# Kernel optimization log

Hardware: AMD Instinct MI355X
Metric: run time of the kernel (lower is better)

The kernel has to match this reference:

```python
import jax, jax.numpy as jnp
import numpy as np

HID, OUT, EMB, NL = 256, 128, 1024, 4
NR, NP_, NM = 16384, 40000, 30000
E = 200000
NTYPES = 3  # lin_nodes keys: protein, molecule, reaction


def setup_inputs() -> dict:
    key = jax.random.key(0)
    ks = jax.random.split(key, 32)
    f32 = jnp.float32
    inp = {}
    inp["x_reaction"] = jax.random.normal(ks[0], (NR, EMB), f32)
    inp["x_protein"] = jax.random.normal(ks[1], (NP_, EMB), f32)
    inp["x_molecule"] = jax.random.normal(ks[2], (NM, EMB), f32)
    inp["ei_p2r_src"] = jax.random.randint(ks[3], (E,), 0, NP_, jnp.int32)
    inp["ei_p2r_dst"] = jax.random.randint(ks[4], (E,), 0, NR, jnp.int32)
    inp["ei_m2r_src"] = jax.random.randint(ks[5], (E,), 0, NM, jnp.int32)
    inp["ei_m2r_dst"] = jax.random.randint(ks[6], (E,), 0, NR, jnp.int32)
    inp["ei_r2p_src"] = jax.random.randint(ks[7], (E,), 0, NR, jnp.int32)
    inp["ei_r2p_dst"] = jax.random.randint(ks[8], (E,), 0, NP_, jnp.int32)
    inp["ei_r2m_src"] = jax.random.randint(ks[9], (E,), 0, NR, jnp.int32)
    inp["ei_r2m_dst"] = jax.random.randint(ks[10], (E,), 0, NM, jnp.int32)
    inp["output_notes_opt"] = jax.random.normal(ks[11], (NR, EMB), f32)
    inp["output_types"] = jax.random.randint(ks[12], (NR,), 0, NTYPES, jnp.int32)
    s = 0.02
    # layer 0 SAGE params (lazy in_dim = EMB), one set per edge type (4 edge types)
    inp["Wl0"] = jax.random.normal(ks[13], (4, EMB, HID), f32) * s
    inp["Wr0"] = jax.random.normal(ks[14], (4, EMB, HID), f32) * s
    inp["bl0"] = jnp.zeros((4, HID), f32)
    # layers 1..3 SAGE params (in_dim = HID)
    inp["Wl"] = jax.random.normal(ks[15], (NL - 1, 4, HID, HID), f32) * s
    inp["Wr"] = jax.random.normal(ks[16], (NL - 1, 4, HID, HID), f32) * s
    inp["bl"] = jnp.zeros((NL - 1, 4, HID), f32)
    inp["W_reaction"] = jax.random.normal(ks[17], (HID, OUT), f32) * s
    inp["b_reaction"] = jnp.zeros((OUT,), f32)
    inp["W_nodes"] = jax.random.normal(ks[18], (NTYPES, EMB, OUT), f32) * s
    inp["b_nodes"] = jnp.zeros((NTYPES, OUT), f32)
    return inp


def _sage(x_src, x_dst, src, dst, n_dst, Wl, bl, Wr):
    # PyG SAGEConv (aggr='mean'): lin_l(mean_{j->i} x_j) + lin_r(x_i); lin_l has bias.
    g = x_src[src]                                              # [E, d] gather
    s = jax.ops.segment_sum(g, dst, num_segments=n_dst)          # [n_dst, d]
    cnt = jax.ops.segment_sum(jnp.ones((src.shape[0],), x_src.dtype), dst, num_segments=n_dst)
    mean = s / jnp.maximum(cnt, 1.0)[:, None]
    return mean @ Wl + bl + x_dst @ Wr


def _hetero_layer(xr, xp, xm, edges, Wl, bl, Wr):
    # HeteroConv(aggr='sum'): sum SAGE outputs per destination node type.
    (ps, pd), (ms, md), (rps, rpd), (rms, rmd) = edges
    new_r = (_sage(xp, xr, ps, pd, NR, Wl[0], bl[0], Wr[0])
             + _sage(xm, xr, ms, md, NR, Wl[1], bl[1], Wr[1]))
    new_p = _sage(xr, xp, rps, rpd, NP_, Wl[2], bl[2], Wr[2])
    new_m = _sage(xr, xm, rms, rmd, NM, Wl[3], bl[3], Wr[3])
    return new_r, new_p, new_m


def reference(x_reaction, x_protein, x_molecule,
              ei_p2r_src, ei_p2r_dst, ei_m2r_src, ei_m2r_dst,
              ei_r2p_src, ei_r2p_dst, ei_r2m_src, ei_r2m_dst,
              output_notes_opt, output_types,
              Wl0, bl0, Wr0, Wl, bl, Wr,
              W_reaction, b_reaction, W_nodes, b_nodes):
    edges = ((ei_p2r_src, ei_p2r_dst), (ei_m2r_src, ei_m2r_dst),
             (ei_r2p_src, ei_r2p_dst), (ei_r2m_src, ei_r2m_dst))
    xr, xp, xm = _hetero_layer(x_reaction, x_protein, x_molecule, edges, Wl0, bl0, Wr0)
    for l in range(NL - 1):
        xr, xp, xm = _hetero_layer(xr, xp, xm, edges, Wl[l], bl[l], Wr[l])
    reaction_out = xr @ W_reaction + b_reaction                  # [NR, OUT]
    # lin_nodes[t](v) per output node: project with all type linears, select by type id
    projs = jnp.einsum('ke,ted->ktd', output_notes_opt, W_nodes) + b_nodes[None]  # [NR, T, OUT]
    node_out = jnp.take_along_axis(projs, output_types[:, None, None].astype(jnp.int32), axis=1)[:, 0, :]
    # cosine similarity along dim=1, torch-style eps clamp on the norm product
    num = jnp.sum(reaction_out * node_out, axis=-1)
    den = jnp.maximum(jnp.linalg.norm(reaction_out, axis=-1) * jnp.linalg.norm(node_out, axis=-1), 1e-8)
    return (num / den + 1.0) * 0.5
```

## Files before the change

### kernel.cpp

```cpp
#include <hip/hip_runtime.h>
#include <math.h>
#include <stdint.h>

#define NR_ 16384
#define NP2_ 40000
#define NM_ 30000
#define NE_ 200000
#define EMB_ 1024
#define HID_ 256
#define OUTD_ 128

typedef __attribute__((ext_vector_type(8))) short bf16x8;
typedef __attribute__((ext_vector_type(4))) float f32x4;
typedef __attribute__((ext_vector_type(8))) unsigned short us8;

__device__ __forceinline__ unsigned short f2bf(float f) {
    uint32_t u = __builtin_bit_cast(uint32_t, f);
    u = (u + 0x7FFFu + ((u >> 16) & 1u)) >> 16;
    return (unsigned short)u;
}
__device__ __forceinline__ float bf2f(unsigned short u) {
    uint32_t v = ((uint32_t)u) << 16;
    return __builtin_bit_cast(float, v);
}

struct Csr4 {
    const int* src[4]; const int* dst[4];
    int* offs[4]; int* cur[4]; int* csr[4];
    int n[4];
};
__global__ void k_zero4(Csr4 c) {
    int y = blockIdx.y;
    int i = blockIdx.x * 256 + threadIdx.x;
    if (i < c.n[y]) c.cur[y][i] = 0;
}
__global__ void k_deg4(Csr4 c) {
    int y = blockIdx.y;
    int i = blockIdx.x * 256 + threadIdx.x;
    if (i < NE_) atomicAdd(&c.cur[y][c.dst[y][i]], 1);
}
__global__ void k_scanA(Csr4 c, int* __restrict__ csum) {
    int y = blockIdx.y;
    int n = c.n[y];
    int ch = blockIdx.x;
    int nch = (n + 1023) >> 10;
    if (ch >= nch) return;
    const int* deg = c.cur[y];
    int* offs = c.offs[y];
    __shared__ int ts[256];
    int base = ch << 10;
    int t = threadIdx.x;
    int v[4];
    int s = 0;
    #pragma unroll
    for (int k = 0; k < 4; ++k) {
        int i = base + t * 4 + k;
        v[k] = (i < n) ? deg[i] : 0;
        s += v[k];
    }
    ts[t] = s;
    __syncthreads();
    for (int st = 1; st < 256; st <<= 1) {
        int x = ts[t];
        int xo = (t >= st) ? ts[t - st] : 0;
        __syncthreads();
        ts[t] = x + xo;
        __syncthreads();
    }
    int run = (t > 0) ? ts[t - 1] : 0;
    #pragma unroll
    for (int k = 0; k < 4; ++k) {
        int i = base + t * 4 + k;
        if (i < n) offs[i] = run;
        run += v[k];
    }
    if (t == 255) csum[y * 40 + ch] = ts[255];
}
__global__ void k_scanB(Csr4 c, int* __restrict__ csum) {
    int y = threadIdx.x;
    if (y < 4) {
        int n = c.n[y];
        int nch = (n + 1023) >> 10;
        int acc = 0;
        for (int i = 0; i < nch; ++i) {
            int v = csum[y * 40 + i];
            csum[y * 40 + i] = acc;
            acc += v;
        }
        c.offs[y][n] = acc;
    }
}
__global__ void k_scanC(Csr4 c, const int* __restrict__ csum) {
    int y = blockIdx.y;
    int i = blockIdx.x * 256 + threadIdx.x;
    if (i < c.n[y]) {
        int v = c.offs[y][i] + csum[y * 40 + (i >> 10)];
        c.offs[y][i] = v;
        c.cur[y][i] = v;
    }
}
__global__ void k_scatter4(Csr4 c) {
    int y = blockIdx.y;
    int i = blockIdx.x * 256 + threadIdx.x;
    if (i < NE_) {
        int d = c.dst[y][i];
        int p = atomicAdd(&c.cur[y][d], 1);
        c.csr[y][p] = c.src[y][i];
    }
}

struct WItem { const float* a; const float* b; unsigned short* dst; int k; int n; };
struct WBatch { WItem it[32]; };
__global__ void k_wconvT(WBatch wb) {
    WItem w = wb.it[blockIdx.y];
    int total = w.k * w.n;
    int kmask = w.k - 1;
    int shift = (w.k == 1024) ? 10 : 8;
    for (int idx = blockIdx.x * 256 + threadIdx.x; idx < total; idx += gridDim.x * 256) {
        int k = idx & kmask, n = idx >> shift;
        float v = w.a[(size_t)k * w.n + n];
        if (w.b) v += w.b[(size_t)k * w.n + n];
        w.dst[idx] = f2bf(v);
    }
}

template <bool OBF, bool AF32>
__global__ __launch_bounds__(256, 3) void k_gemm(
    const void* __restrict__ Av, int lda,
    const unsigned short* __restrict__ Bt,
    void* __restrict__ Cv, int ldc, const float* __restrict__ bias,
    int M, int K)
{
    __shared__ __align__(16) unsigned short As[128 * 64];
    __shared__ __align__(16) unsigned short Bs[128 * 64];
    const int tid = threadIdx.x;
    const int lane = tid & 63;
    int nwg = gridDim.x * gridDim.y;
    int o = blockIdx.y * gridDim.x + blockIdx.x;
    int q = nwg >> 3, r = nwg & 7;
    int xcd = o & 7, j = o >> 3;
    int wg = (xcd < r ? xcd * (q + 1) : r * (q + 1) + (xcd - r) * q) + j;
    const int bm = (wg / gridDim.y) * 128;
    const int bn = (wg % gridDim.y) * 128;
    const int wave = tid >> 6;
    const int wr = (wave >> 1) * 64;
    const int wc = (wave & 1) * 64;
    const int frow = lane & 15;
    const int fkc = lane >> 4;
    f32x4 acc[4][4] = {};

    for (int k0 = 0; k0 < K; k0 += 64) {
        #pragma unroll
        for (int i = 0; i < 4; ++i) {
            int c = tid + i * 256;
            int row = c >> 3, kc = c & 7;
            int srck = k0 + ((kc ^ (row & 7)) << 3);
            int ga = min(bm + row, M - 1);
            if constexpr (AF32) {
                const float* Af = (const float*)Av + (size_t)ga * lda + srck;
                float4 a0 = *(const float4*)Af;
                float4 a1 = *(const float4*)(Af + 4);
                us8 oo;
                oo[0] = f2bf(a0.x); oo[1] = f2bf(a0.y); oo[2] = f2bf(a0.z); oo[3] = f2bf(a0.w);
                oo[4] = f2bf(a1.x); oo[5] = f2bf(a1.y); oo[6] = f2bf(a1.z); oo[7] = f2bf(a1.w);
                *(us8*)(As + (size_t)c * 8) = oo;
            } else {
                __builtin_amdgcn_global_load_lds(
                    (const __attribute__((address_space(1))) unsigned int*)((const unsigned short*)Av + (size_t)ga * lda + srck),
                    (__attribute__((address_space(3))) unsigned int*)(As + (size_t)c * 8), 16, 0, 0);
            }
            __builtin_amdgcn_global_load_lds(
                (const __attribute__((address_space(1))) unsigned int*)(Bt + (size_t)(bn + row) * K + srck),
                (__attribute__((address_space(3))) unsigned int*)(Bs + (size_t)c * 8), 16, 0, 0);
        }
        __syncthreads();
        #pragma unroll
        for (int kk = 0; kk < 2; ++kk) {
            bf16x8 af[4], bfr[4];
            #pragma unroll
            for (int m = 0; m < 4; ++m) {
                int row = wr + m * 16 + frow;
                int kc = kk * 4 + fkc;
                af[m] = *(const bf16x8*)(As + (size_t)((row << 3) + (kc ^ (row & 7))) * 8);
            }
            #pragma unroll
            for (int n = 0; n < 4; ++n) {
                int row = wc + n * 16 + frow;
                int kc = kk * 4 + fkc;
                bfr[n] = *(const bf16x8*)(Bs + (size_t)((row << 3) + (kc ^ (row & 7))) * 8);
            }
            #pragma unroll
            for (int m = 0; m < 4; ++m)
                #pragma unroll
                for (int n = 0; n < 4; ++n)
                    acc[m][n] = __builtin_amdgcn_mfma_f32_16x16x32_bf16(bfr[n], af[m], acc[m][n], 0, 0, 0);
        }
        __syncthreads();
    }

    const int ccol0 = (lane >> 4) << 2;
    #pragma unroll
    for (int m = 0; m < 4; ++m) {
        int row = bm + wr + m * 16 + frow;
        if (row < M) {
            #pragma unroll
            for (int n = 0; n < 4; ++n) {
                int col = bn + wc + n * 16 + ccol0;
                f32x4 v = acc[m][n];
                if (bias) {
                    v[0] += bias[col + 0];
                    v[1] += bias[col + 1];
                    v[2] += bias[col + 2];
                    v[3] += bias[col + 3];
                }
                if constexpr (OBF) {
                    ushort4 oo;
                    oo.x = f2bf(v[0]); oo.y = f2bf(v[1]); oo.z = f2bf(v[2]); oo.w = f2bf(v[3]);
                    *(ushort4*)((unsigned short*)Cv + (size_t)row * ldc + col) = oo;
                } else {
                    *(float4*)((float*)Cv + (size_t)row * ldc + col) = make_float4(v[0], v[1], v[2], v[3]);
                }
            }
        }
    }
}

__global__ __launch_bounds__(256) void k_aggw(const int* __restrict__ offs,
                                              const int* __restrict__ csr,
                                              const unsigned short* __restrict__ proj, int ldp,
                                              const float* __restrict__ bias,
                                              unsigned short* __restrict__ outx, int ldo,
                                              int ndst) {
    int node = blockIdx.x * 4 + (threadIdx.x >> 6);
    int lane = threadIdx.x & 63;
    if (node >= ndst) return;
    int beg = offs[node], end = offs[node + 1];
    float s0 = 0.f, s1 = 0.f, s2 = 0.f, s3 = 0.f;
    const unsigned short* base = proj + lane * 4;
    int e = beg;
    for (; e + 1 < end; e += 2) {
        int i0 = csr[e], i1 = csr[e + 1];
        ushort4 u0 = *(const ushort4*)(base + (size_t)i0 * ldp);
        ushort4 u1 = *(const ushort4*)(base + (size_t)i1 * ldp);
        s0 += bf2f(u0.x) + bf2f(u1.x);
        s1 += bf2f(u0.y) + bf2f(u1.y);
        s2 += bf2f(u0.z) + bf2f(u1.z);
        s3 += bf2f(u0.w) + bf2f(u1.w);
    }
    if (e < end) {
        ushort4 u = *(const ushort4*)(base + (size_t)csr[e] * ldp);
        s0 += bf2f(u.x); s1 += bf2f(u.y); s2 += bf2f(u.z); s3 += bf2f(u.w);
    }
    float inv = 1.f / fmaxf((float)(end - beg), 1.f);
    float4 b4 = ((const float4*)bias)[lane];
    size_t o = (size_t)node * ldo + lane * 4;
    ushort4 cur = *(const ushort4*)(outx + o);
    ushort4 w;
    w.x = f2bf(bf2f(cur.x) + s0 * inv + b4.x);
    w.y = f2bf(bf2f(cur.y) + s1 * inv + b4.y);
    w.z = f2bf(bf2f(cur.z) + s2 * inv + b4.z);
    w.w = f2bf(bf2f(cur.w) + s3 * inv + b4.w);
    *(ushort4*)(outx + o) = w;
}

__global__ __launch_bounds__(256) void k_agg2w(const int* __restrict__ offsA,
                                               const int* __restrict__ csrA,
                                               const unsigned short* __restrict__ projA, int ldpA,
                                               const float* __restrict__ biasA,
                                               const int* __restrict__ offsB,
                                               const int* __restrict__ csrB,
                                               const unsigned short* __restrict__ projB, int ldpB,
                                               const float* __restrict__ biasB,
                                               unsigned short* __restrict__ outx, int ldo,
                                               int ndst) {
    int node = blockIdx.x * 4 + (threadIdx.x >> 6);
    int lane = threadIdx.x & 63;
    if (node >= ndst) return;
    float a0 = 0.f, a1 = 0.f, a2 = 0.f, a3 = 0.f;
    int begA = offsA[node], endA = offsA[node + 1];
    const unsigned short* baseA = projA + lane * 4;
    int e = begA;
    for (; e + 1 < endA; e += 2) {
        int i0 = csrA[e], i1 = csrA[e + 1];
        ushort4 u0 = *(const ushort4*)(baseA + (size_t)i0 * ldpA);
        ushort4 u1 = *(const ushort4*)(baseA + (size_t)i1 * ldpA);
        a0 += bf2f(u0.x) + bf2f(u1.x);
        a1 += bf2f(u0.y) + bf2f(u1.y);
        a2 += bf2f(u0.z) + bf2f(u1.z);
        a3 += bf2f(u0.w) + bf2f(u1.w);
    }
    if (e < endA) {
        ushort4 u = *(const ushort4*)(baseA + (size_t)csrA[e] * ldpA);
        a0 += bf2f(u.x); a1 += bf2f(u.y); a2 += bf2f(u.z); a3 += bf2f(u.w);
    }
    float b0 = 0.f, b1 = 0.f, b2 = 0.f, b3 = 0.f;
    int begB = offsB[node], endB = offsB[node + 1];
    const unsigned short* baseB = projB + lane * 4;
    e = begB;
    for (; e + 1 < endB; e += 2) {
        int i0 = csrB[e], i1 = csrB[e + 1];
        ushort4 u0 = *(const ushort4*)(baseB + (size_t)i0 * ldpB);
        ushort4 u1 = *(const ushort4*)(baseB + (size_t)i1 * ldpB);
        b0 += bf2f(u0.x) + bf2f(u1.x);
        b1 += bf2f(u0.y) + bf2f(u1.y);
        b2 += bf2f(u0.z) + bf2f(u1.z);
        b3 += bf2f(u0.w) + bf2f(u1.w);
    }
    if (e < endB) {
        ushort4 u = *(const ushort4*)(baseB + (size_t)csrB[e] * ldpB);
        b0 += bf2f(u.x); b1 += bf2f(u.y); b2 += bf2f(u.z); b3 += bf2f(u.w);
    }
    float invA = 1.f / fmaxf((float)(endA - begA), 1.f);
    float invB = 1.f / fmaxf((float)(endB - begB), 1.f);
    float4 bA = ((const float4*)biasA)[lane];
    float4 bB = ((const float4*)biasB)[lane];
    size_t o = (size_t)node * ldo + lane * 4;
    ushort4 cur = *(const ushort4*)(outx + o);
    ushort4 w;
    w.x = f2bf(bf2f(cur.x) + a0 * invA + bA.x + b0 * invB + bB.x);
    w.y = f2bf(bf2f(cur.y) + a1 * invA + bA.y + b1 * invB + bB.y);
    w.z = f2bf(bf2f(cur.z) + a2 * invA + bA.z + b2 * invB + bB.z);
    w.w = f2bf(bf2f(cur.w) + a3 * invA + bA.w + b3 * invB + bB.w);
    *(ushort4*)(outx + o) = w;
}

__global__ __launch_bounds__(256) void k_cos(const float* __restrict__ ro,
                                             const float* __restrict__ pr,
                                             const int* __restrict__ types,
                                             float* __restrict__ out, int nr) {
    int row = blockIdx.x * 4 + (threadIdx.x >> 6);
    int lane = threadIdx.x & 63;
    if (row >= nr) return;
    int t = types[row];
    float2 r = ((const float2*)(ro + (size_t)row * OUTD_))[lane];
    float2 nn = ((const float2*)(pr + (size_t)row * 384 + t * OUTD_))[lane];
    float num = r.x * nn.x + r.y * nn.y;
    float d1 = r.x * r.x + r.y * r.y;
    float d2 = nn.x * nn.x + nn.y * nn.y;
    #pragma unroll
    for (int s = 1; s < 64; s <<= 1) {
        num += __shfl_xor(num, s);
        d1 += __shfl_xor(d1, s);
        d2 += __shfl_xor(d2, s);
    }
    if (lane == 0) out[row] = (num / fmaxf(sqrtf(d1) * sqrtf(d2), 1e-8f) + 1.f) * 0.5f;
}

extern "C" void kernel_launch(void* const* d_in, const int* in_sizes, int n_in,
                              void* d_out, int out_size, void* d_ws, size_t ws_size,
                              hipStream_t stream) {
    const float* x_r0 = (const float*)d_in[0];
    const float* x_p0 = (const float*)d_in[1];
    const float* x_m0 = (const float*)d_in[2];
    const int* e_src[4] = {(const int*)d_in[3], (const int*)d_in[5], (const int*)d_in[7], (const int*)d_in[9]};
    const int* e_dst[4] = {(const int*)d_in[4], (const int*)d_in[6], (const int*)d_in[8], (const int*)d_in[10]};
    const float* notes = (const float*)d_in[11];
    const int* types = (const int*)d_in[12];
    const float* Wl0 = (const float*)d_in[13];
    const float* Wr0 = (const float*)d_in[14];
    const float* bl0 = (const float*)d_in[15];
    const float* WlL = (const float*)d_in[16];
    const float* WrL = (const float*)d_in[17];
    const float* blL = (const float*)d_in[18];
    const float* Wre = (const float*)d_in[19];
    const float* bre = (const float*)d_in[20];
    const float* Wn  = (const float*)d_in[21];
    const float* bn  = (const float*)d_in[22];
    float* out = (float*)d_out;

    uintptr_t base = (uintptr_t)d_ws;
    auto alloc = [&](size_t bytes) -> void* {
        uintptr_t p = (base + 255) & ~(uintptr_t)255;
        base = p + bytes;
        return (void*)p;
    };
    unsigned short* Rb[2] = {(unsigned short*)alloc((size_t)NR_ * 768 * 2),
                             (unsigned short*)alloc((size_t)NR_ * 768 * 2)};
    unsigned short* Pb[2] = {(unsigned short*)alloc((size_t)NP2_ * 512 * 2),
                             (unsigned short*)alloc((size_t)NP2_ * 512 * 2)};
    unsigned short* Mb[2] = {(unsigned short*)alloc((size_t)NM_ * 512 * 2),
                             (unsigned short*)alloc((size_t)NM_ * 512 * 2)};
    float* ro = (float*)alloc((size_t)NR_ * OUTD_ * 4);
    float* pr = (float*)alloc((size_t)NR_ * 384 * 4);
    unsigned short* wbf = (unsigned short*)alloc((size_t)4000000 * 2);
    int* csum = (int*)alloc(160 * 4);
    int nd[4] = {NR_, NR_, NP2_, NM_};
    Csr4 cs{};
    for (int t = 0; t < 4; ++t) {
        cs.src[t] = e_src[t]; cs.dst[t] = e_dst[t]; cs.n[t] = nd[t];
        cs.offs[t] = (int*)alloc(((size_t)nd[t] + 1) * 4);
        cs.cur[t]  = (int*)alloc((size_t)nd[t] * 4);
        cs.csr[t]  = (int*)alloc((size_t)NE_ * 4);
    }

    unsigned short *BR[4], *BP[4], *BM[4], *Bre, *Bn;
    {
        WBatch wb{};
        int cnt = 0;
        size_t woff = 0;
        auto add = [&](const float* a, const float* bb, int K, int N) -> unsigned short* {
            unsigned short* dst = wbf + woff;
            woff += (size_t)K * N;
            wb.it[cnt] = WItem{a, bb, dst, K, N};
            ++cnt;
            return dst;
        };
        const size_t w0 = (size_t)EMB_ * HID_;
        const size_t wl = (size_t)HID_ * HID_;
        for (int l = 0; l < 4; ++l) {
            int K = (l == 0) ? EMB_ : HID_;
            const float* Wr_ = (l == 0) ? Wr0 : WrL + (size_t)(l - 1) * 4 * wl;
            const float* Wl_ = (l == 0) ? Wl0 : WlL + (size_t)(l - 1) * 4 * wl;
            size_t ws_ = (l == 0) ? w0 : wl;
            BR[l] = add(Wr_ + 0 * ws_, Wr_ + 1 * ws_, K, HID_);
            add(Wl_ + 2 * ws_, nullptr, K, HID_);
            add(Wl_ + 3 * ws_, nullptr, K, HID_);
            BP[l] = add(Wr_ + 2 * ws_, nullptr, K, HID_);
            add(Wl_ + 0 * ws_, nullptr, K, HID_);
            BM[l] = add(Wr_ + 3 * ws_, nullptr, K, HID_);
            add(Wl_ + 1 * ws_, nullptr, K, HID_);
        }
        Bre = add(Wre, nullptr, HID_, OUTD_);
        Bn = add(Wn + 0 * (size_t)EMB_ * OUTD_, nullptr, EMB_, OUTD_);
        add(Wn + 1 * (size_t)EMB_ * OUTD_, nullptr, EMB_, OUTD_);
        add(Wn + 2 * (size_t)EMB_ * OUTD_, nullptr, EMB_, OUTD_);
        k_wconvT<<<dim3(128, cnt), 256, 0, stream>>>(wb);
    }

    k_zero4<<<dim3((NP2_ + 255) / 256, 4), 256, 0, stream>>>(cs);
    k_deg4<<<dim3((NE_ + 255) / 256, 4), 256, 0, stream>>>(cs);
    k_scanA<<<dim3(40, 4), 256, 0, stream>>>(cs, csum);
    k_scanB<<<1, 64, 0, stream>>>(cs, csum);
    k_scanC<<<dim3((NP2_ + 255) / 256, 4), 256, 0, stream>>>(cs, csum);
    k_scatter4<<<dim3((NE_ + 255) / 256, 4), 256, 0, stream>>>(cs);

    auto gemm_bf = [&](const unsigned short* A, int lda, const unsigned short* Bt,
                       unsigned short* C, int ldc, int M, int N, int K) {
        k_gemm<true, false><<<dim3((M + 127) / 128, N / 128), 256, 0, stream>>>(
            A, lda, Bt, C, ldc, nullptr, M, K);
    };
    auto gemm_f32a_bf = [&](const float* A, int lda, const unsigned short* Bt,
                            unsigned short* C, int ldc, int M, int N, int K) {
        k_gemm<true, true><<<dim3((M + 127) / 128, N / 128), 256, 0, stream>>>(
            A, lda, Bt, C, ldc, nullptr, M, K);
    };

    for (int l = 0; l < 4; ++l) {
        int K = (l == 0) ? EMB_ : HID_;
        unsigned short* R = Rb[l & 1];
        unsigned short* P = Pb[l & 1];
        unsigned short* M = Mb[l & 1];
        const float* bl_ = (l == 0) ? bl0 : blL + (size_t)(l - 1) * 4 * HID_;

        if (l == 0) {
            gemm_f32a_bf(x_r0, EMB_, BR[0], R, 768, NR_, 768, EMB_);
            gemm_f32a_bf(x_p0, EMB_, BP[0], P, 512, NP2_, 512, EMB_);
            gemm_f32a_bf(x_m0, EMB_, BM[0], M, 512, NM_, 512, EMB_);
        } else {
            gemm_bf(Rb[(l - 1) & 1], 768, BR[l], R, 768, NR_, 768, K);
            gemm_bf(Pb[(l - 1) & 1], 512, BP[l], P, 512, NP2_, 512, K);
            gemm_bf(Mb[(l - 1) & 1], 512, BM[l], M, 512, NM_, 512, K);
        }

        k_agg2w<<<(NR_ + 3) / 4, 256, 0, stream>>>(cs.offs[0], cs.csr[0], P + 256, 512, bl_ + 0 * HID_,
                                                   cs.offs[1], cs.csr[1], M + 256, 512, bl_ + 1 * HID_,
                                                   R, 768, NR_);
        k_aggw<<<(NP2_ + 3) / 4, 256, 0, stream>>>(cs.offs[2], cs.csr[2], R + 256, 768, bl_ + 2 * HID_, P, 512, NP2_);
        k_aggw<<<(NM_ + 3) / 4, 256, 0, stream>>>(cs.offs[3], cs.csr[3], R + 512, 768, bl_ + 3 * HID_, M, 512, NM_);
    }

    k_gemm<false, false><<<dim3((NR_ + 127) / 128, 1), 256, 0, stream>>>(
        Rb[1], 768, Bre, ro, OUTD_, bre, NR_, HID_);
    k_gemm<false, true><<<dim3((NR_ + 127) / 128, 3), 256, 0, stream>>>(
        notes, EMB_, Bn, pr, 384, bn, NR_, EMB_);
    k_cos<<<NR_ / 4, 256, 0, stream>>>(ro, pr, types, out, NR_);
}
```

Measured before the change: 887.9 us.

## Double-buffer LDS tiles in GEMM to overlap global loads with MFMA

The GEMM kernel now keeps two LDS buffers for the A and B tiles and prefetches the next K-tile while running MFMAs on the current one. This removes one barrier per iteration. For fp32 A inputs, the next tile is loaded into registers and converted to bf16 after the compute step. This doubles LDS use to 64KB and lowers the launch-bounds occupancy hint from 3 to 2 blocks, trading occupancy and register pressure for overlap.

New measurement: 936.2 us. 1.05x slower.

```diff
diff --git a/kernel.cpp b/kernel.cpp
--- a/kernel.cpp
+++ b/kernel.cpp
@@ -125,14 +125,14 @@
 }
 
 template <bool OBF, bool AF32>
-__global__ __launch_bounds__(256, 3) void k_gemm(
+__global__ __launch_bounds__(256, 2) void k_gemm(
     const void* __restrict__ Av, int lda,
     const unsigned short* __restrict__ Bt,
     void* __restrict__ Cv, int ldc, const float* __restrict__ bias,
     int M, int K)
 {
-    __shared__ __align__(16) unsigned short As[128 * 64];
-    __shared__ __align__(16) unsigned short Bs[128 * 64];
+    __shared__ __align__(16) unsigned short As[2][128 * 64];
+    __shared__ __align__(16) unsigned short Bs[2][128 * 64];
     const int tid = threadIdx.x;
     const int lane = tid & 63;
     int nwg = gridDim.x * gridDim.y;
@@ -148,54 +148,104 @@
     const int frow = lane & 15;
     const int fkc = lane >> 4;
     f32x4 acc[4][4] = {};
-
-    for (int k0 = 0; k0 < K; k0 += 64) {
-        #pragma unroll
-        for (int i = 0; i < 4; ++i) {
-            int c = tid + i * 256;
-            int row = c >> 3, kc = c & 7;
-            int srck = k0 + ((kc ^ (row & 7)) << 3);
-            int ga = min(bm + row, M - 1);
-            if constexpr (AF32) {
-                const float* Af = (const float*)Av + (size_t)ga * lda + srck;
-                float4 a0 = *(const float4*)Af;
-                float4 a1 = *(const float4*)(Af + 4);
-                us8 oo;
-                oo[0] = f2bf(a0.x); oo[1] = f2bf(a0.y); oo[2] = f2bf(a0.z); oo[3] = f2bf(a0.w);
-                oo[4] = f2bf(a1.x); oo[5] = f2bf(a1.y); oo[6] = f2bf(a1.z); oo[7] = f2bf(a1.w);
-                *(us8*)(As + (size_t)c * 8) = oo;
-            } else {
-                __builtin_amdgcn_global_load_lds(
-                    (const __attribute__((address_space(1))) unsigned int*)((const unsigned short*)Av + (size_t)ga * lda + srck),
-                    (__attribute__((address_space(3))) unsigned int*)(As + (size_t)c * 8), 16, 0, 0);
+    float4 ra0[4], ra1[4];
+    (void)ra0; (void)ra1;
+
+#define STAGE_AB(bufi, kk0) do {                                                           \
+    _Pragma("unroll")                                                                      \
+    for (int i = 0; i < 4; ++i) {                                                          \
+        int c = tid + i * 256, rw = c >> 3, kc = c & 7;                                    \
+        int srck = (kk0) + ((kc ^ (rw & 7)) << 3);                                         \
+        int ga = min(bm + rw, M - 1);                                                      \
+        __builtin_amdgcn_global_load_lds(                                                  \
+            (const __attribute__((address_space(1))) unsigned int*)((const unsigned short*)Av + (size_t)ga * lda + srck), \
+            (__attribute__((address_space(3))) unsigned int*)(&As[bufi][c * 8]), 16, 0, 0);\
+        __builtin_amdgcn_global_load_lds(                                                  \
+            (const __attribute__((address_space(1))) unsigned int*)(Bt + (size_t)(bn + rw) * K + srck), \
+            (__attribute__((address_space(3))) unsigned int*)(&Bs[bufi][c * 8]), 16, 0, 0);\
+    } } while (0)
+
+#define ALOAD(kk0) do {                                                                    \
+    _Pragma("unroll")                                                                      \
+    for (int i = 0; i < 4; ++i) {                                                          \
+        int c = tid + i * 256, rw = c >> 3, kc = c & 7;                                    \
+        int srck = (kk0) + ((kc ^ (rw & 7)) << 3);                                         \
+        int ga = min(bm + rw, M - 1);                                                      \
+        const float* Af = (const float*)Av + (size_t)ga * lda + srck;                      \
+        ra0[i] = *(const float4*)Af;                                                       \
+        ra1[i] = *(const float4*)(Af + 4);                                                 \
+    } } while (0)
+
+#define AWRITE(bufi) do {                                                                  \
+    _Pragma("unroll")                                                                      \
+    for (int i = 0; i < 4; ++i) {                                                          \
+        int c = tid + i * 256;                                                             \
+        us8 oo;                                                                            \
+        oo[0] = f2bf(ra0[i].x); oo[1] = f2bf(ra0[i].y);                                    \
+        oo[2] = f2bf(ra0[i].z); oo[3] = f2bf(ra0[i].w);                                    \
+        oo[4] = f2bf(ra1[i].x); oo[5] = f2bf(ra1[i].y);                                    \
+        oo[6] = f2bf(ra1[i].z); oo[7] = f2bf(ra1[i].w);                                    \
+        *(us8*)(&As[bufi][c * 8]) = oo;                                                    \
+    } } while (0)
+
+#define STAGE_B(bufi, kk0) do {                                                            \
+    _Pragma("unroll")                                                                      \
+    for (int i = 0; i < 4; ++i) {                                                          \
+        int c = tid + i * 256, rw = c >> 3, kc = c & 7;                                    \
+        int srck = (kk0) + ((kc ^ (rw & 7)) << 3);                                         \
+        __builtin_amdgcn_global_load_lds(                                                  \
+            (const __attribute__((address_space(1))) unsigned int*)(Bt + (size_t)(bn + rw) * K + srck), \
+            (__attribute__((address_space(3))) unsigned int*)(&Bs[bufi][c * 8]), 16, 0, 0);\
+    } } while (0)
+
+#define COMPUTE(bufi) do {                                                                 \
+    _Pragma("unroll")                                                                      \
+    for (int kk = 0; kk < 2; ++kk) {                                                       \
+        bf16x8 af[4], bfr[4];                                                              \
+        _Pragma("unroll")                                                                  \
+        for (int m = 0; m < 4; ++m) {                                                      \
+            int rw = wr + m * 16 + frow;                                                   \
+            int kc = kk * 4 + fkc;                                                         \
+            af[m] = *(const bf16x8*)(&As[bufi][((rw << 3) + (kc ^ (rw & 7))) * 8]);        \
+        }                                                                                  \
+        _Pragma("unroll")                                                                  \
+        for (int n = 0; n < 4; ++n) {                                                      \
+            int rw = wc + n * 16 + frow;                                                   \
+            int kc = kk * 4 + fkc;                                                         \
+            bfr[n] = *(const bf16x8*)(&Bs[bufi][((rw << 3) + (kc ^ (rw & 7))) * 8]);       \
+        }                                                                                  \
+        _Pragma("unroll")                                                                  \
+        for (int m = 0; m < 4; ++m)                                                        \
+            _Pragma("unroll")                                                              \
+            for (int n = 0; n < 4; ++n)                                                    \
+                acc[m][n] = __builtin_amdgcn_mfma_f32_16x16x32_bf16(bfr[n], af[m], acc[m][n], 0, 0, 0); \
+    } } while (0)
+
+    const int nt = K >> 6;
+    if constexpr (AF32) {
+        ALOAD(0);
+        STAGE_B(0, 0);
+        AWRITE(0);
+        __syncthreads();
+        for (int t = 0; t < nt; ++t) {
+            int bufi = t & 1;
+            if (t + 1 < nt) {
+                ALOAD((t + 1) << 6);
+                STAGE_B(bufi ^ 1, (t + 1) << 6);
             }
-            __builtin_amdgcn_global_load_lds(
-                (const __attribute__((address_space(1))) unsigned int*)(Bt + (size_t)(bn + row) * K + srck),
-                (__attribute__((address_space(3))) unsigned int*)(Bs + (size_t)c * 8), 16, 0, 0);
+            COMPUTE(bufi);
+            if (t + 1 < nt) AWRITE(bufi ^ 1);
+            __syncthreads();
         }
+    } else {
+        STAGE_AB(0, 0);
         __syncthreads();
-        #pragma unroll
-        for (int kk = 0; kk < 2; ++kk) {
-            bf16x8 af[4], bfr[4];
-            #pragma unroll
-            for (int m = 0; m < 4; ++m) {
-                int row = wr + m * 16 + frow;
-                int kc = kk * 4 + fkc;
-                af[m] = *(const bf16x8*)(As + (size_t)((row << 3) + (kc ^ (row & 7))) * 8);
-            }
-            #pragma unroll
-            for (int n = 0; n < 4; ++n) {
-                int row = wc + n * 16 + frow;
-                int kc = kk * 4 + fkc;
-                bfr[n] = *(const bf16x8*)(Bs + (size_t)((row << 3) + (kc ^ (row & 7))) * 8);
-            }
-            #pragma unroll
-            for (int m = 0; m < 4; ++m)
-                #pragma unroll
-                for (int n = 0; n < 4; ++n)
-                    acc[m][n] = __builtin_amdgcn_mfma_f32_16x16x32_bf16(bfr[n], af[m], acc[m][n], 0, 0, 0);
+        for (int t = 0; t < nt; ++t) {
+            int bufi = t & 1;
+            if (t + 1 < nt) STAGE_AB(bufi ^ 1, (t + 1) << 6);
+            COMPUTE(bufi);
+            __syncthreads();
         }
-        __syncthreads();
     }
 
     const int ccol0 = (lane >> 4) << 2;
@@ -223,6 +273,11 @@
             }
         }
     }
+#undef STAGE_AB
+#undef ALOAD
+#undef AWRITE
+#undef STAGE_B
+#undef COMPUTE
 }
 
 __global__ __launch_bounds__(256) void k_aggw(const int* __restrict__ offs,
```

## Batch per-layer node-type GEMMs into one grouped launch; unroll aggregation gathers by four

Applied to the files above, without the earlier changes.

The three per-layer projection GEMMs (reaction, protein, molecule) are merged into one grouped kernel. It takes a segment table and maps each workgroup to its segment through block-offset thresholds, which removes two launches per layer and lets tail tiles of one GEMM overlap with the next. The CSR mean-aggregation loops are also unrolled from two to four gathers per iteration so more loads are in flight. The cost is extra per-block segment selection and struct reads, and higher register use in the aggregation kernels.

Result: faster. 805.5 us (-9.3%).

```diff
diff --git a/kernel.cpp b/kernel.cpp
--- a/kernel.cpp
+++ b/kernel.cpp
@@ -124,24 +124,32 @@
     }
 }
 
+struct GSeg {
+    const void* A; const unsigned short* Bt; void* C; const float* bias;
+    int lda, ldc, M, K, ntn, blk0;
+};
+struct GBatch { GSeg s[3]; int b1, b2, tot; };
+
 template <bool OBF, bool AF32>
-__global__ __launch_bounds__(256, 3) void k_gemm(
-    const void* __restrict__ Av, int lda,
-    const unsigned short* __restrict__ Bt,
-    void* __restrict__ Cv, int ldc, const float* __restrict__ bias,
-    int M, int K)
-{
+__global__ __launch_bounds__(256, 3) void k_gemmb(GBatch gb) {
     __shared__ __align__(16) unsigned short As[128 * 64];
     __shared__ __align__(16) unsigned short Bs[128 * 64];
     const int tid = threadIdx.x;
     const int lane = tid & 63;
-    int nwg = gridDim.x * gridDim.y;
-    int o = blockIdx.y * gridDim.x + blockIdx.x;
+    int nwg = gb.tot;
+    int o = blockIdx.x;
     int q = nwg >> 3, r = nwg & 7;
     int xcd = o & 7, j = o >> 3;
     int wg = (xcd < r ? xcd * (q + 1) : r * (q + 1) + (xcd - r) * q) + j;
-    const int bm = (wg / gridDim.y) * 128;
-    const int bn = (wg % gridDim.y) * 128;
+    const int si = (wg >= gb.b1) + (wg >= gb.b2);
+    const GSeg sg = gb.s[si];
+    const int local = wg - sg.blk0;
+    const int bm = (local / sg.ntn) * 128;
+    const int bn = (local % sg.ntn) * 128;
+    const int lda = sg.lda, ldc = sg.ldc, M = sg.M, K = sg.K;
+    const unsigned short* __restrict__ Bt = sg.Bt;
+    const float* __restrict__ bias = sg.bias;
+
     const int wave = tid >> 6;
     const int wr = (wave >> 1) * 64;
     const int wc = (wave & 1) * 64;
@@ -157,7 +165,7 @@
             int srck = k0 + ((kc ^ (row & 7)) << 3);
             int ga = min(bm + row, M - 1);
             if constexpr (AF32) {
-                const float* Af = (const float*)Av + (size_t)ga * lda + srck;
+                const float* Af = (const float*)sg.A + (size_t)ga * lda + srck;
                 float4 a0 = *(const float4*)Af;
                 float4 a1 = *(const float4*)(Af + 4);
                 us8 oo;
@@ -166,7 +174,7 @@
                 *(us8*)(As + (size_t)c * 8) = oo;
             } else {
                 __builtin_amdgcn_global_load_lds(
-                    (const __attribute__((address_space(1))) unsigned int*)((const unsigned short*)Av + (size_t)ga * lda + srck),
+                    (const __attribute__((address_space(1))) unsigned int*)((const unsigned short*)sg.A + (size_t)ga * lda + srck),
                     (__attribute__((address_space(3))) unsigned int*)(As + (size_t)c * 8), 16, 0, 0);
             }
             __builtin_amdgcn_global_load_lds(
@@ -216,9 +224,9 @@
                 if constexpr (OBF) {
                     ushort4 oo;
                     oo.x = f2bf(v[0]); oo.y = f2bf(v[1]); oo.z = f2bf(v[2]); oo.w = f2bf(v[3]);
-                    *(ushort4*)((unsigned short*)Cv + (size_t)row * ldc + col) = oo;
+                    *(ushort4*)((unsigned short*)sg.C + (size_t)row * ldc + col) = oo;
                 } else {
-                    *(float4*)((float*)Cv + (size_t)row * ldc + col) = make_float4(v[0], v[1], v[2], v[3]);
+                    *(float4*)((float*)sg.C + (size_t)row * ldc + col) = make_float4(v[0], v[1], v[2], v[3]);
                 }
             }
         }
@@ -238,16 +246,18 @@
     float s0 = 0.f, s1 = 0.f, s2 = 0.f, s3 = 0.f;
     const unsigned short* base = proj + lane * 4;
     int e = beg;
-    for (; e + 1 < end; e += 2) {
-        int i0 = csr[e], i1 = csr[e + 1];
+    for (; e + 3 < end; e += 4) {
+        int i0 = csr[e], i1 = csr[e + 1], i2 = csr[e + 2], i3 = csr[e + 3];
         ushort4 u0 = *(const ushort4*)(base + (size_t)i0 * ldp);
         ushort4 u1 = *(const ushort4*)(base + (size_t)i1 * ldp);
-        s0 += bf2f(u0.x) + bf2f(u1.x);
-        s1 += bf2f(u0.y) + bf2f(u1.y);
-        s2 += bf2f(u0.z) + bf2f(u1.z);
-        s3 += bf2f(u0.w) + bf2f(u1.w);
-    }
-    if (e < end) {
+        ushort4 u2 = *(const ushort4*)(base + (size_t)i2 * ldp);
+        ushort4 u3 = *(const ushort4*)(base + (size_t)i3 * ldp);
+        s0 += bf2f(u0.x) + bf2f(u1.x) + bf2f(u2.x) + bf2f(u3.x);
+        s1 += bf2f(u0.y) + bf2f(u1.y) + bf2f(u2.y) + bf2f(u3.y);
+        s2 += bf2f(u0.z) + bf2f(u1.z) + bf2f(u2.z) + bf2f(u3.z);
+        s3 += bf2f(u0.w) + bf2f(u1.w) + bf2f(u2.w) + bf2f(u3.w);
+    }
+    for (; e < end; ++e) {
         ushort4 u = *(const ushort4*)(base + (size_t)csr[e] * ldp);
         s0 += bf2f(u.x); s1 += bf2f(u.y); s2 += bf2f(u.z); s3 += bf2f(u.w);
     }
@@ -280,16 +290,18 @@
     int begA = offsA[node], endA = offsA[node + 1];
     const unsigned short* baseA = projA + lane * 4;
     int e = begA;
-    for (; e + 1 < endA; e += 2) {
-        int i0 = csrA[e], i1 = csrA[e + 1];
+    for (; e + 3 < endA; e += 4) {
+        int i0 = csrA[e], i1 = csrA[e + 1], i2 = csrA[e + 2], i3 = csrA[e + 3];
         ushort4 u0 = *(const ushort4*)(baseA + (size_t)i0 * ldpA);
         ushort4 u1 = *(const ushort4*)(baseA + (size_t)i1 * ldpA);
-        a0 += bf2f(u0.x) + bf2f(u1.x);
-        a1 += bf2f(u0.y) + bf2f(u1.y);
-        a2 += bf2f(u0.z) + bf2f(u1.z);
-        a3 += bf2f(u0.w) + bf2f(u1.w);
-    }
-    if (e < endA) {
+        ushort4 u2 = *(const ushort4*)(baseA + (size_t)i2 * ldpA);
+        ushort4 u3 = *(const ushort4*)(baseA + (size_t)i3 * ldpA);
+        a0 += bf2f(u0.x) + bf2f(u1.x) + bf2f(u2.x) + bf2f(u3.x);
+        a1 += bf2f(u0.y) + bf2f(u1.y) + bf2f(u2.y) + bf2f(u3.y);
+        a2 += bf2f(u0.z) + bf2f(u1.z) + bf2f(u2.z) + bf2f(u3.z);
+        a3 += bf2f(u0.w) + bf2f(u1.w) + bf2f(u2.w) + bf2f(u3.w);
+    }
+    for (; e < endA; ++e) {
         ushort4 u = *(const ushort4*)(baseA + (size_t)csrA[e] * ldpA);
         a0 += bf2f(u.x); a1 += bf2f(u.y); a2 += bf2f(u.z); a3 += bf2f(u.w);
     }
@@ -297,16 +309,18 @@
     int begB = offsB[node], endB = offsB[node + 1];
     const unsigned short* baseB = projB + lane * 4;
     e = begB;
-    for (; e + 1 < endB; e += 2) {
-        int i0 = csrB[e], i1 = csrB[e + 1];
+    for (; e + 3 < endB; e += 4) {
+        int i0 = csrB[e], i1 = csrB[e + 1], i2 = csrB[e + 2], i3 = csrB[e + 3];
         ushort4 u0 = *(const ushort4*)(baseB + (size_t)i0 * ldpB);
         ushort4 u1 = *(const ushort4*)(baseB + (size_t)i1 * ldpB);
-        b0 += bf2f(u0.x) + bf2f(u1.x);
-        b1 += bf2f(u0.y) + bf2f(u1.y);
-        b2 += bf2f(u0.z) + bf2f(u1.z);
-        b3 += bf2f(u0.w) + bf2f(u1.w);
-    }
-    if (e < endB) {
+        ushort4 u2 = *(const ushort4*)(baseB + (size_t)i2 * ldpB);
+        ushort4 u3 = *(const ushort4*)(baseB + (size_t)i3 * ldpB);
+        b0 += bf2f(u0.x) + bf2f(u1.x) + bf2f(u2.x) + bf2f(u3.x);
+        b1 += bf2f(u0.y) + bf2f(u1.y) + bf2f(u2.y) + bf2f(u3.y);
+        b2 += bf2f(u0.z) + bf2f(u1.z) + bf2f(u2.z) + bf2f(u3.z);
+        b3 += bf2f(u0.w) + bf2f(u1.w) + bf2f(u2.w) + bf2f(u3.w);
+    }
+    for (; e < endB; ++e) {
         ushort4 u = *(const ushort4*)(baseB + (size_t)csrB[e] * ldpB);
         b0 += bf2f(u.x); b1 += bf2f(u.y); b2 += bf2f(u.z); b3 += bf2f(u.w);
     }
@@ -434,15 +448,12 @@
     k_scanC<<<dim3((NP2_ + 255) / 256, 4), 256, 0, stream>>>(cs, csum);
     k_scatter4<<<dim3((NE_ + 255) / 256, 4), 256, 0, stream>>>(cs);
 
-    auto gemm_bf = [&](const unsigned short* A, int lda, const unsigned short* Bt,
-                       unsigned short* C, int ldc, int M, int N, int K) {
-        k_gemm<true, false><<<dim3((M + 127) / 128, N / 128), 256, 0, stream>>>(
-            A, lda, Bt, C, ldc, nullptr, M, K);
-    };
-    auto gemm_f32a_bf = [&](const float* A, int lda, const unsigned short* Bt,
-                            unsigned short* C, int ldc, int M, int N, int K) {
-        k_gemm<true, true><<<dim3((M + 127) / 128, N / 128), 256, 0, stream>>>(
-            A, lda, Bt, C, ldc, nullptr, M, K);
+    const int MT_R = (NR_ + 127) / 128;
+    const int MT_P = (NP2_ + 127) / 128;
+    const int MT_M = (NM_ + 127) / 128;
+    auto seg = [](const void* A, const unsigned short* Bt, void* C, const float* bias,
+                  int lda, int ldc, int M, int K, int ntn, int blk0) -> GSeg {
+        return GSeg{A, Bt, C, bias, lda, ldc, M, K, ntn, blk0};
     };
 
     for (int l = 0; l < 4; ++l) {
@@ -452,15 +463,20 @@
         unsigned short* M = Mb[l & 1];
         const float* bl_ = (l == 0) ? bl0 : blL + (size_t)(l - 1) * 4 * HID_;
 
+        GBatch gb{};
+        int nR = MT_R * 6, nP = MT_P * 4, nM = MT_M * 4;
         if (l == 0) {
-            gemm_f32a_bf(x_r0, EMB_, BR[0], R, 768, NR_, 768, EMB_);
-            gemm_f32a_bf(x_p0, EMB_, BP[0], P, 512, NP2_, 512, EMB_);
-            gemm_f32a_bf(x_m0, EMB_, BM[0], M, 512, NM_, 512, EMB_);
+            gb.s[0] = seg(x_r0, BR[0], R, nullptr, EMB_, 768, NR_, EMB_, 6, 0);
+            gb.s[1] = seg(x_p0, BP[0], P, nullptr, EMB_, 512, NP2_, EMB_, 4, nR);
+            gb.s[2] = seg(x_m0, BM[0], M, nullptr, EMB_, 512, NM_, EMB_, 4, nR + nP);
         } else {
-            gemm_bf(Rb[(l - 1) & 1], 768, BR[l], R, 768, NR_, 768, K);
-            gemm_bf(Pb[(l - 1) & 1], 512, BP[l], P, 512, NP2_, 512, K);
-            gemm_bf(Mb[(l - 1) & 1], 512, BM[l], M, 512, NM_, 512, K);
-        }
+            gb.s[0] = seg(Rb[(l - 1) & 1], BR[l], R, nullptr, 768, 768, NR_, K, 6, 0);
+            gb.s[1] = seg(Pb[(l - 1) & 1], BP[l], P, nullptr, 512, 512, NP2_, K, 4, nR);
+            gb.s[2] = seg(Mb[(l - 1) & 1], BM[l], M, nullptr, 512, 512, NM_, K, 4, nR + nP);
+        }
+        gb.b1 = nR; gb.b2 = nR + nP; gb.tot = nR + nP + nM;
+        if (l == 0) k_gemmb<true, true><<<gb.tot, 256, 0, stream>>>(gb);
+        else        k_gemmb<true, false><<<gb.tot, 256, 0, stream>>>(gb);
 
         k_agg2w<<<(NR_ + 3) / 4, 256, 0, stream>>>(cs.offs[0], cs.csr[0], P + 256, 512, bl_ + 0 * HID_,
                                                    cs.offs[1], cs.csr[1], M + 256, 512, bl_ + 1 * HID_,
@@ -469,9 +485,15 @@
         k_aggw<<<(NM_ + 3) / 4, 256, 0, stream>>>(cs.offs[3], cs.csr[3], R + 512, 768, bl_ + 3 * HID_, M, 512, NM_);
     }
 
-    k_gemm<false, false><<<dim3((NR_ + 127) / 128, 1), 256, 0, stream>>>(
-        Rb[1], 768, Bre, ro, OUTD_, bre, NR_, HID_);
-    k_gemm<false, true><<<dim3((NR_ + 127) / 128, 3), 256, 0, stream>>>(
-        notes, EMB_, Bn, pr, 384, bn, NR_, EMB_);
+    {
+        GBatch g1{};
+        g1.s[0] = seg(Rb[1], Bre, ro, bre, 768, OUTD_, NR_, HID_, 1, 0);
+        g1.b1 = g1.b2 = g1.tot = MT_R * 1;
+        k_gemmb<false, false><<<g1.tot, 256, 0, stream>>>(g1);
+        GBatch g2{};
+        g2.s[0] = seg(notes, Bn, pr, bn, EMB_, 384, NR_, EMB_, 3, 0);
+        g2.b1 = g2.b2 = g2.tot = MT_R * 3;
+        k_gemmb<false, true><<<g2.tot, 256, 0, stream>>>(g2);
+    }
     k_cos<<<NR_ / 4, 256, 0, stream>>>(ro, pr, types, out, NR_);
 }
```
